# Optimization experiments

Hardware: AMD Instinct MI355X
Metric: run time of the kernel (lower is better)

Reference implementation:

```python
import jax, jax.numpy as jnp
import numpy as np

HEADS = 8
DIM_HEAD = 40
SCALE = DIM_HEAD ** -0.5


def setup_inputs() -> dict:
    key = jax.random.key(0)
    ks = jax.random.split(key, 6)
    B, S, D = 2, 4096, 320  # batch, seq (64x64 latent), query_dim
    inner = HEADS * DIM_HEAD  # 320
    s = 0.02
    return {
        "x": jax.random.normal(ks[0], (B, S, D), jnp.float32),
        "Wq": jax.random.normal(ks[1], (inner, D), jnp.float32) * s,
        "Wk": jax.random.normal(ks[2], (inner, D), jnp.float32) * s,
        "Wv": jax.random.normal(ks[3], (inner, D), jnp.float32) * s,
        "Wout": jax.random.normal(ks[4], (D, inner), jnp.float32) * s,
        "bout": jnp.zeros((D,), jnp.float32),
    }


def _split_heads(t):
    # [B, S, h*d] -> [B, h, S, d]
    B, S, _ = t.shape
    return t.reshape(B, S, HEADS, DIM_HEAD).transpose(0, 2, 1, 3)


def reference(x, Wq, Wk, Wv, Wout, bout):
    # self-attention path (context=None): k/v come from x
    q = _split_heads(x @ Wq.T)  # [B,h,S,d]
    k = _split_heads(x @ Wk.T)
    v = _split_heads(x @ Wv.T)
    # scores: materialized O(S^2) attention as in the torch einsum
    attn = jax.nn.softmax(jnp.einsum('bhid,bhjd->bhij', q, k) * SCALE, axis=-1)
    out = jnp.einsum('bhij,bhjd->bhid', attn, v)  # [B,h,S,d]
    B, _, S, _ = out.shape
    out = out.transpose(0, 2, 1, 3).reshape(B, S, HEADS * DIM_HEAD)
    return out @ Wout.T + bout  # to_out (dropout=0 -> identity)
```

## Files before the change

kernel.cpp:

```cpp
#include <hip/hip_runtime.h>

#define HEADS 8
#define DHEAD 40
#define SEQ   4096
#define BATCH 2
#define INNER 320
#define NBH   16
#define QSCALE ((float)(0.15811388300841897 * 1.4426950408889634))

typedef _Float16 f16;
typedef __attribute__((ext_vector_type(2)))  __fp16   fp16x2;
typedef __attribute__((ext_vector_type(4)))  _Float16 half4;
typedef __attribute__((ext_vector_type(8)))  _Float16 half8;
typedef __attribute__((ext_vector_type(16))) float    f32x16;

#if __has_builtin(__builtin_amdgcn_exp2f)
#define EXP2F(x) __builtin_amdgcn_exp2f(x)
#else
#define EXP2F(x) exp2f(x)
#endif

#define MFMA16(a, b, c) __builtin_amdgcn_mfma_f32_32x32x16_f16(a, b, c, 0, 0, 0)

union H8 { half8 h8; fp16x2 p2[4]; uint4 u4; };

#define WQKV4 (3 * INNER * INNER / 4)
#define WOUT4 (INNER * INNER / 4)
#define WTOT4 (WQKV4 + WOUT4)

__global__ __launch_bounds__(256)
void convert_kernel(const float* __restrict__ Wq,
                    const float* __restrict__ Wk,
                    const float* __restrict__ Wv,
                    const float* __restrict__ Wout,
                    f16* __restrict__ wh, f16* __restrict__ wouth)
{
    int i = blockIdx.x * 256 + threadIdx.x;
    if (i >= WTOT4) return;
    float4 v;
    f16* dst;
    float sc = 1.0f;
    if (i < WQKV4) {
        if (i < 25600)      { v = ((const float4*)Wq)[i]; sc = QSCALE; }
        else if (i < 51200) { v = ((const float4*)Wk)[i - 25600]; }
        else                { v = ((const float4*)Wv)[i - 51200]; }
        dst = wh + 4 * (size_t)i;
    } else {
        int j = i - WQKV4;
        v = ((const float4*)Wout)[j];
        dst = wouth + 4 * (size_t)j;
    }
    H8 u;
    u.p2[0] = __builtin_amdgcn_cvt_pkrtz(v.x * sc, v.y * sc);
    u.p2[1] = __builtin_amdgcn_cvt_pkrtz(v.z * sc, v.w * sc);
    *(uint2*)dst = make_uint2(u.u4.x, u.u4.y);
}

#define QSTR 72

__global__ __launch_bounds__(256)
void qkv_gemm_kernel(const float* __restrict__ x, const f16* __restrict__ wh,
                     f16* __restrict__ q, f16* __restrict__ k,
                     f16* __restrict__ vt)
{
    __shared__ f16 lds[(64 + 192) * QSTR];
    f16* As = lds;
    f16* Bs = lds + 64 * QSTR;

    const int tid = threadIdx.x;
    const int nb0 = blockIdx.x * 64;
    const int m0  = blockIdx.y * 64;
    const int wave = tid >> 6, lane = tid & 63, m = lane & 31, half = lane >> 5;
    const int mw = wave >> 1, nw = wave & 1;

    f32x16 acc[3];
    #pragma unroll
    for (int i = 0; i < 16; i++) { acc[0][i] = 0.f; acc[1][i] = 0.f; acc[2][i] = 0.f; }

    for (int k0 = 0; k0 < 320; k0 += 64) {
        __syncthreads();
        #pragma unroll
        for (int u = 0; u < 2; u++) {
            int idx = tid + 256 * u;
            int r = idx >> 3, c8 = idx & 7;
            const float* xr = &x[(size_t)(m0 + r) * 320 + k0 + c8 * 8];
            float4 v0 = *(const float4*)xr;
            float4 v1 = *(const float4*)(xr + 4);
            H8 hh;
            hh.p2[0] = __builtin_amdgcn_cvt_pkrtz(v0.x, v0.y);
            hh.p2[1] = __builtin_amdgcn_cvt_pkrtz(v0.z, v0.w);
            hh.p2[2] = __builtin_amdgcn_cvt_pkrtz(v1.x, v1.y);
            hh.p2[3] = __builtin_amdgcn_cvt_pkrtz(v1.z, v1.w);
            *(uint4*)&As[r * QSTR + c8 * 8] = hh.u4;
        }
        #pragma unroll
        for (int u = 0; u < 6; u++) {
            int idx = tid + 256 * u;
            int r = idx >> 3, c8 = idx & 7;
            int wr = (r >> 6) * 320 + nb0 + (r & 63);
            *(uint4*)&Bs[r * QSTR + c8 * 8] =
                *(const uint4*)&wh[(size_t)wr * 320 + k0 + c8 * 8];
        }
        __syncthreads();
        #pragma unroll
        for (int c = 0; c < 4; c++) {
            half8 a = *(const half8*)&As[(mw * 32 + m) * QSTR + c * 16 + half * 8];
            #pragma unroll
            for (int t = 0; t < 3; t++) {
                half8 bf = *(const half8*)&Bs[(nw * 96 + t * 32 + m) * QSTR + c * 16 + half * 8];
                acc[t] = MFMA16(a, bf, acc[t]);
            }
        }
    }

    const int b = m0 >> 12, s0 = m0 & 4095;

    #pragma unroll
    for (int t = 0; t < 3; t++) {
        int st = nw * 3 + t;
        if (st < 4) {
            f16* dst = (st < 2) ? q : k;
            int col = nb0 + (st & 1) * 32 + m;
            int h  = (col * 205) >> 13;
            int dd = col - h * 40;
            #pragma unroll
            for (int reg = 0; reg < 16; reg++) {
                int crow = 4 * half + (reg & 3) + 8 * (reg >> 2);
                int mg = m0 + mw * 32 + crow;
                int bb = mg >> 12, s = mg & 4095;
                dst[((size_t)(bb * 8 + h) * SEQ + s) * DHEAD + dd] = (f16)acc[t][reg];
            }
        }
    }

    __syncthreads();
    f16* Ct = lds;
    if (nw == 1) {
        #pragma unroll
        for (int t = 1; t < 3; t++) {
            int vr0 = (t - 1) * 32 + m;
            #pragma unroll
            for (int g = 0; g < 4; g++) {
                half4 hh;
                hh.x = (f16)acc[t][4 * g + 0]; hh.y = (f16)acc[t][4 * g + 1];
                hh.z = (f16)acc[t][4 * g + 2]; hh.w = (f16)acc[t][4 * g + 3];
                *(half4*)&Ct[vr0 * QSTR + mw * 32 + 8 * g + 4 * half] = hh;
            }
        }
    }
    __syncthreads();
    #pragma unroll
    for (int u = 0; u < 4; u++) {
        int idx = tid + 256 * u;
        int rl = idx >> 4, c4 = idx & 15;
        int col = nb0 + rl;
        int h  = (col * 205) >> 13;
        int dd = col - h * 40;
        int w4 = c4 & 3;
        int c4p = (c4 & ~3) | ((w4 == 1) ? 2 : (w4 == 2) ? 1 : w4);
        *(uint2*)&vt[((size_t)(b * 8 + h) * DHEAD + dd) * SEQ + s0 + c4p * 4] =
            *(const uint2*)&Ct[rl * QSTR + c4 * 4];
    }
}

__global__ __launch_bounds__(512, 4)
void attn_kernel(const f16* __restrict__ q, const f16* __restrict__ k,
                 const f16* __restrict__ vt, f16* __restrict__ y)
{
    __shared__ __align__(16) unsigned char ldsbuf[49152];
    f16*   ldsh = (f16*)ldsbuf;
    float* ldsf = (float*)ldsbuf;

    const int tid = threadIdx.x;
    const int blk = blockIdx.x;
    const int xcd = blk & 7, slot = blk >> 3;
    const int bh = xcd * 2 + (slot >> 5), qt = slot & 31;
    const int b = bh >> 3, h = bh & 7;
    const int q0 = qt * 128;
    const int wave = tid >> 6, lane = tid & 63, m = lane & 31, half = lane >> 5;
    const int qp = wave >> 1, kh = wave & 1;
    const int x7 = m & 7;

    if (tid < 192) {
        int bsel = tid >> 6, r = tid & 63;
        *(uint4*)&ldsh[bsel * 8192 + r * 64 + 8 * (5 ^ (r & 7))] = make_uint4(0, 0, 0, 0);
    }
    {
        int idx = tid;
        #pragma unroll
        for (int pass = 0; pass < 2; pass++) {
            if (pass == 0 || tid < 64) {
                int bsel = idx / 192;
                int j = idx - bsel * 192;
                int r = 40 + (j >> 3), c = j & 7;
                uint4 val = (r == 40) ? make_uint4(0x3C003C00u, 0x3C003C00u, 0x3C003C00u, 0x3C003C00u)
                                      : make_uint4(0, 0, 0, 0);
                *(uint4*)&ldsh[bsel * 8192 + 4096 + r * 64 + 8 * (c ^ (r & 7))] = val;
            }
            idx = 512 + tid;
        }
    }

    half8 zero8;
    #pragma unroll
    for (int j = 0; j < 8; j++) zero8[j] = (f16)0.0f;

    half8 qa[3];
    {
        const f16* qb = q + ((size_t)bh * SEQ + q0 + qp * 32 + m) * DHEAD;
        qa[0] = *(const half8*)&qb[half * 8];
        qa[1] = *(const half8*)&qb[16 + half * 8];
        qa[2] = (half == 1) ? zero8 : *(const half8*)&qb[32];
    }

    f32x16 O0, O1;
    #pragma unroll
    for (int i = 0; i < 16; i++) { O0[i] = 0.f; O1[i] = 0.f; }

    const f16* kb = k  + (size_t)bh * SEQ * DHEAD;
    const f16* vb = vt + (size_t)bh * DHEAD * SEQ;

    const bool aIsK = (tid < 320);
    int adst, astep;
    const f16* aptr;
    if (aIsK) {
        int r = (tid * 205) >> 10, c = tid - r * 5;
        adst = r * 64 + 8 * (c ^ (r & 7));
        aptr = kb + (size_t)r * DHEAD + c * 8;
        astep = 64 * DHEAD;
    } else {
        int t = tid - 320;
        int r = t >> 3, c = t & 7;
        adst = 4096 + r * 64 + 8 * (c ^ (r & 7));
        aptr = vb + (size_t)r * SEQ + c * 8;
        astep = 64;
    }
    const bool hasB = (tid < 128);
    int bdst = 0;
    const f16* bptr = vb;
    if (hasB) {
        int t = 192 + tid;
        int r = t >> 3, c = t & 7;
        bdst = 4096 + r * 64 + 8 * (c ^ (r & 7));
        bptr = vb + (size_t)r * SEQ + c * 8;
    }

    uint4 sA = *(const uint4*)aptr;
    uint4 sB = make_uint4(0, 0, 0, 0);
    if (hasB) sB = *(const uint4*)bptr;

    H8 p0, p1;
    int stg  = 0;
    int stgv = 0;

    {
        *(uint4*)&ldsh[stg + adst] = sA;
        if (hasB) *(uint4*)&ldsh[stg + bdst] = sB;
        __syncthreads();
        aptr += astep; sA = *(const uint4*)aptr;
        if (hasB) { bptr += 64; sB = *(const uint4*)bptr; }

        half8 kf[3];
        #pragma unroll
        for (int c = 0; c < 3; c++)
            kf[c] = *(const half8*)&ldsh[stg + (kh * 32 + m) * 64 + 8 * ((2 * c + half) ^ x7)];
        f32x16 S;
        #pragma unroll
        for (int i = 0; i < 16; i++) S[i] = 0.f;
        __builtin_amdgcn_s_setprio(1);
        S = MFMA16(kf[0], qa[0], S);
        S = MFMA16(kf[1], qa[1], S);
        S = MFMA16(kf[2], qa[2], S);
        __builtin_amdgcn_s_setprio(0);
        #pragma unroll
        for (int g = 0; g < 4; g++) {
            p0.p2[g] = __builtin_amdgcn_cvt_pkrtz(EXP2F(S[2 * g]),     EXP2F(S[2 * g + 1]));
            p1.p2[g] = __builtin_amdgcn_cvt_pkrtz(EXP2F(S[8 + 2 * g]), EXP2F(S[9 + 2 * g]));
        }
        stg = 8192;
    }

    for (int j = 1; j < 64; ++j) {
        *(uint4*)&ldsh[stg + adst] = sA;
        if (hasB) *(uint4*)&ldsh[stg + bdst] = sB;

        {
            const f16* Vb = &ldsh[stgv + 4096];
            half8 vf[2][2];
            #pragma unroll
            for (int c = 0; c < 2; c++) {
                vf[c][0] = *(const half8*)&Vb[m * 64        + 8 * ((4 * kh + 2 * c + half) ^ x7)];
                vf[c][1] = *(const half8*)&Vb[(32 + m) * 64 + 8 * ((4 * kh + 2 * c + half) ^ x7)];
            }
            __builtin_amdgcn_s_setprio(1);
            O0 = MFMA16(p0.h8, vf[0][0], O0);
            O1 = MFMA16(p0.h8, vf[0][1], O1);
            O0 = MFMA16(p1.h8, vf[1][0], O0);
            O1 = MFMA16(p1.h8, vf[1][1], O1);
            __builtin_amdgcn_s_setprio(0);
        }

        __syncthreads();

        if (j < 63) {
            aptr += astep; sA = *(const uint4*)aptr;
            if (hasB) { bptr += 64; sB = *(const uint4*)bptr; }
        }

        half8 kf[3];
        #pragma unroll
        for (int c = 0; c < 3; c++)
            kf[c] = *(const half8*)&ldsh[stg + (kh * 32 + m) * 64 + 8 * ((2 * c + half) ^ x7)];
        f32x16 S;
        #pragma unroll
        for (int i = 0; i < 16; i++) S[i] = 0.f;
        __builtin_amdgcn_s_setprio(1);
        S = MFMA16(kf[0], qa[0], S);
        S = MFMA16(kf[1], qa[1], S);
        S = MFMA16(kf[2], qa[2], S);
        __builtin_amdgcn_s_setprio(0);

        #pragma unroll
        for (int g = 0; g < 4; g++) {
            p0.p2[g] = __builtin_amdgcn_cvt_pkrtz(EXP2F(S[2 * g]),     EXP2F(S[2 * g + 1]));
            p1.p2[g] = __builtin_amdgcn_cvt_pkrtz(EXP2F(S[8 + 2 * g]), EXP2F(S[9 + 2 * g]));
        }

        stgv = stg;
        stg = (stg == 16384) ? 0 : stg + 8192;
    }

    {
        const f16* Vb = &ldsh[stgv + 4096];
        half8 vf[2][2];
        #pragma unroll
        for (int c = 0; c < 2; c++) {
            vf[c][0] = *(const half8*)&Vb[m * 64        + 8 * ((4 * kh + 2 * c + half) ^ x7)];
            vf[c][1] = *(const half8*)&Vb[(32 + m) * 64 + 8 * ((4 * kh + 2 * c + half) ^ x7)];
        }
        O0 = MFMA16(p0.h8, vf[0][0], O0);
        O1 = MFMA16(p0.h8, vf[0][1], O1);
        O0 = MFMA16(p1.h8, vf[1][0], O0);
        O1 = MFMA16(p1.h8, vf[1][1], O1);
    }

    __syncthreads();
    if (kh == 1) {
        #pragma unroll
        for (int reg = 0; reg < 16; reg++) {
            int row = 4 * half + (reg & 3) + 8 * (reg >> 2);
            ldsf[(qp * 32 + row) * 66 + m]      = O0[reg];
            ldsf[(qp * 32 + row) * 66 + 32 + m] = O1[reg];
        }
    }
    __syncthreads();
    if (kh == 0) {
        #pragma unroll
        for (int reg = 0; reg < 16; reg++) {
            int row = 4 * half + (reg & 3) + 8 * (reg >> 2);
            O0[reg] += ldsf[(qp * 32 + row) * 66 + m];
            O1[reg] += ldsf[(qp * 32 + row) * 66 + 32 + m];
        }
        #pragma unroll
        for (int reg = 0; reg < 16; reg++) {
            float l = __shfl(O1[reg], 8 + 32 * half, 64);
            float rinv = 1.0f / l;
            int row = 4 * half + (reg & 3) + 8 * (reg >> 2);
            f16* yr = y + ((size_t)b * SEQ + q0 + qp * 32 + row) * INNER + h * DHEAD;
            yr[m] = (f16)(O0[reg] * rinv);
            if (m < 8) yr[32 + m] = (f16)(O1[reg] * rinv);
        }
    }
}

#define ASTR 72

__global__ __launch_bounds__(256)
void out_proj_kernel(const f16* __restrict__ y, const f16* __restrict__ wouth,
                     const float* __restrict__ bout, float* __restrict__ out)
{
    __shared__ f16 lds[(128 + 64) * ASTR];
    f16* As = lds;
    f16* Bs = lds + 128 * ASTR;

    const int tid = threadIdx.x;
    const int m0 = blockIdx.y * 128;
    const int n0 = blockIdx.x * 64;
    const int wave = tid >> 6, lane = tid & 63, m = lane & 31, half = lane >> 5;

    f32x16 acc[2];
    #pragma unroll
    for (int i = 0; i < 16; i++) { acc[0][i] = 0.f; acc[1][i] = 0.f; }

    for (int k0 = 0; k0 < 320; k0 += 64) {
        __syncthreads();
        #pragma unroll
        for (int u = 0; u < 4; u++) {
            int idx = tid + 256 * u;
            int r = idx >> 3, c8 = idx & 7;
            *(uint4*)&As[r * ASTR + c8 * 8] =
                *(const uint4*)&y[(size_t)(m0 + r) * 320 + k0 + c8 * 8];
        }
        #pragma unroll
        for (int u = 0; u < 2; u++) {
            int idx = tid + 256 * u;
            int r = idx >> 3, c8 = idx & 7;
            *(uint4*)&Bs[r * ASTR + c8 * 8] =
                *(const uint4*)&wouth[(size_t)(n0 + r) * 320 + k0 + c8 * 8];
        }
        __syncthreads();
        #pragma unroll
        for (int c = 0; c < 4; c++) {
            half8 a  = *(const half8*)&As[(wave * 32 + m) * ASTR + c * 16 + half * 8];
            half8 b0 = *(const half8*)&Bs[m * ASTR + c * 16 + half * 8];
            half8 b1 = *(const half8*)&Bs[(32 + m) * ASTR + c * 16 + half * 8];
            acc[0] = MFMA16(a, b0, acc[0]);
            acc[1] = MFMA16(a, b1, acc[1]);
        }
    }

    #pragma unroll
    for (int nt = 0; nt < 2; nt++) {
        int n = n0 + nt * 32 + m;
        float bias = bout[n];
        #pragma unroll
        for (int reg = 0; reg < 16; reg++) {
            int crow = 4 * half + (reg & 3) + 8 * (reg >> 2);
            out[(size_t)(m0 + wave * 32 + crow) * 320 + n] = acc[nt][reg] + bias;
        }
    }
}

extern "C" void kernel_launch(void* const* d_in, const int* in_sizes, int n_in,
                              void* d_out, int out_size, void* d_ws, size_t ws_size,
                              hipStream_t stream)
{
    const float* x    = (const float*)d_in[0];
    const float* Wq   = (const float*)d_in[1];
    const float* Wk   = (const float*)d_in[2];
    const float* Wv   = (const float*)d_in[3];
    const float* Wout = (const float*)d_in[4];
    const float* bout = (const float*)d_in[5];
    float* out = (float*)d_out;

    unsigned char* ws = (unsigned char*)d_ws;
    f16* wh    = (f16*)(ws);
    f16* wouth = (f16*)(ws +   614400);
    f16* qd    = (f16*)(ws +   819200);
    f16* kd    = (f16*)(ws +  6062080);
    f16* vtd   = (f16*)(ws + 11304960);
    f16* yd    = (f16*)(ws + 16547840);

    convert_kernel <<<400,          256, 0, stream>>>(Wq, Wk, Wv, Wout, wh, wouth);
    qkv_gemm_kernel<<<dim3(5, 128), 256, 0, stream>>>(x, wh, qd, kd, vtd);
    attn_kernel    <<<512,          512, 0, stream>>>(qd, kd, vtd, yd);
    out_proj_kernel<<<dim3(5, 64),  256, 0, stream>>>(yd, wouth, bout, out);
}
```

Measured before the change: 159.5 us.

## Fuse weight fp16 conversion into GEMM loaders and reorder attention loop

Removes the separate weight conversion kernel; the QKV and output projection GEMMs now load fp32 weights and convert to fp16 (with Q scaling) while staging into LDS. This drops one kernel launch and a workspace round-trip, but each block redundantly converts weights and reads twice the weight bytes. The attention main loop is reordered so the barrier follows the K/V store immediately and the QK^T MFMAs for the new tile are issued before the PV MFMAs of the previous tile, aiming to improve MFMA/exp overlap.

```diff
diff --git a/kernel.cpp b/kernel.cpp
--- a/kernel.cpp
+++ b/kernel.cpp
@@ -24,42 +24,24 @@
 
 union H8 { half8 h8; fp16x2 p2[4]; uint4 u4; };
 
-#define WQKV4 (3 * INNER * INNER / 4)
-#define WOUT4 (INNER * INNER / 4)
-#define WTOT4 (WQKV4 + WOUT4)
+static __device__ __forceinline__ uint4 cvt8(const float* __restrict__ p, float sc) {
+    float4 v0 = *(const float4*)p;
+    float4 v1 = *(const float4*)(p + 4);
+    H8 hh;
+    hh.p2[0] = __builtin_amdgcn_cvt_pkrtz(v0.x * sc, v0.y * sc);
+    hh.p2[1] = __builtin_amdgcn_cvt_pkrtz(v0.z * sc, v0.w * sc);
+    hh.p2[2] = __builtin_amdgcn_cvt_pkrtz(v1.x * sc, v1.y * sc);
+    hh.p2[3] = __builtin_amdgcn_cvt_pkrtz(v1.z * sc, v1.w * sc);
+    return hh.u4;
+}
+
+#define QSTR 72
 
 __global__ __launch_bounds__(256)
-void convert_kernel(const float* __restrict__ Wq,
-                    const float* __restrict__ Wk,
-                    const float* __restrict__ Wv,
-                    const float* __restrict__ Wout,
-                    f16* __restrict__ wh, f16* __restrict__ wouth)
-{
-    int i = blockIdx.x * 256 + threadIdx.x;
-    if (i >= WTOT4) return;
-    float4 v;
-    f16* dst;
-    float sc = 1.0f;
-    if (i < WQKV4) {
-        if (i < 25600)      { v = ((const float4*)Wq)[i]; sc = QSCALE; }
-        else if (i < 51200) { v = ((const float4*)Wk)[i - 25600]; }
-        else                { v = ((const float4*)Wv)[i - 51200]; }
-        dst = wh + 4 * (size_t)i;
-    } else {
-        int j = i - WQKV4;
-        v = ((const float4*)Wout)[j];
-        dst = wouth + 4 * (size_t)j;
-    }
-    H8 u;
-    u.p2[0] = __builtin_amdgcn_cvt_pkrtz(v.x * sc, v.y * sc);
-    u.p2[1] = __builtin_amdgcn_cvt_pkrtz(v.z * sc, v.w * sc);
-    *(uint2*)dst = make_uint2(u.u4.x, u.u4.y);
-}
-
-#define QSTR 72
-
-__global__ __launch_bounds__(256)
-void qkv_gemm_kernel(const float* __restrict__ x, const f16* __restrict__ wh,
+void qkv_gemm_kernel(const float* __restrict__ x,
+                     const float* __restrict__ Wq,
+                     const float* __restrict__ Wk,
+                     const float* __restrict__ Wv,
                      f16* __restrict__ q, f16* __restrict__ k,
                      f16* __restrict__ vt)
 {
@@ -73,6 +55,18 @@
     const int wave = tid >> 6, lane = tid & 63, m = lane & 31, half = lane >> 5;
     const int mw = wave >> 1, nw = wave & 1;
 
+    const int bc8 = tid & 7;
+    const float* bsrc[6];
+    int bdst[6];
+    #pragma unroll
+    for (int u = 0; u < 6; u++) {
+        int idx = tid + 256 * u;
+        int r = idx >> 3;
+        const float* W = (r < 64) ? Wq : (r < 128) ? Wk : Wv;
+        bsrc[u] = W + (size_t)(nb0 + (r & 63)) * 320 + bc8 * 8;
+        bdst[u] = r * QSTR + bc8 * 8;
+    }
+
     f32x16 acc[3];
     #pragma unroll
     for (int i = 0; i < 16; i++) { acc[0][i] = 0.f; acc[1][i] = 0.f; acc[2][i] = 0.f; }
@@ -83,24 +77,12 @@
         for (int u = 0; u < 2; u++) {
             int idx = tid + 256 * u;
             int r = idx >> 3, c8 = idx & 7;
-            const float* xr = &x[(size_t)(m0 + r) * 320 + k0 + c8 * 8];
-            float4 v0 = *(const float4*)xr;
-            float4 v1 = *(const float4*)(xr + 4);
-            H8 hh;
-            hh.p2[0] = __builtin_amdgcn_cvt_pkrtz(v0.x, v0.y);
-            hh.p2[1] = __builtin_amdgcn_cvt_pkrtz(v0.z, v0.w);
-            hh.p2[2] = __builtin_amdgcn_cvt_pkrtz(v1.x, v1.y);
-            hh.p2[3] = __builtin_amdgcn_cvt_pkrtz(v1.z, v1.w);
-            *(uint4*)&As[r * QSTR + c8 * 8] = hh.u4;
-        }
-        #pragma unroll
-        for (int u = 0; u < 6; u++) {
-            int idx = tid + 256 * u;
-            int r = idx >> 3, c8 = idx & 7;
-            int wr = (r >> 6) * 320 + nb0 + (r & 63);
-            *(uint4*)&Bs[r * QSTR + c8 * 8] =
-                *(const uint4*)&wh[(size_t)wr * 320 + k0 + c8 * 8];
-        }
+            *(uint4*)&As[r * QSTR + c8 * 8] =
+                cvt8(&x[(size_t)(m0 + r) * 320 + k0 + c8 * 8], 1.0f);
+        }
+        #pragma unroll
+        for (int u = 0; u < 6; u++)
+            *(uint4*)&Bs[bdst[u]] = cvt8(bsrc[u] + k0, (u < 2) ? QSCALE : 1.0f);
         __syncthreads();
         #pragma unroll
         for (int c = 0; c < 4; c++) {
@@ -283,6 +265,25 @@
     for (int j = 1; j < 64; ++j) {
         *(uint4*)&ldsh[stg + adst] = sA;
         if (hasB) *(uint4*)&ldsh[stg + bdst] = sB;
+        __syncthreads();
+
+        if (j < 63) {
+            aptr += astep; sA = *(const uint4*)aptr;
+            if (hasB) { bptr += 64; sB = *(const uint4*)bptr; }
+        }
+
+        half8 kf[3];
+        #pragma unroll
+        for (int c = 0; c < 3; c++)
+            kf[c] = *(const half8*)&ldsh[stg + (kh * 32 + m) * 64 + 8 * ((2 * c + half) ^ x7)];
+        f32x16 S;
+        #pragma unroll
+        for (int i = 0; i < 16; i++) S[i] = 0.f;
+        __builtin_amdgcn_s_setprio(1);
+        S = MFMA16(kf[0], qa[0], S);
+        S = MFMA16(kf[1], qa[1], S);
+        S = MFMA16(kf[2], qa[2], S);
+        __builtin_amdgcn_s_setprio(0);
 
         {
             const f16* Vb = &ldsh[stgv + 4096];
@@ -300,26 +301,6 @@
             __builtin_amdgcn_s_setprio(0);
         }
 
-        __syncthreads();
-
-        if (j < 63) {
-            aptr += astep; sA = *(const uint4*)aptr;
-            if (hasB) { bptr += 64; sB = *(const uint4*)bptr; }
-        }
-
-        half8 kf[3];
-        #pragma unroll
-        for (int c = 0; c < 3; c++)
-            kf[c] = *(const half8*)&ldsh[stg + (kh * 32 + m) * 64 + 8 * ((2 * c + half) ^ x7)];
-        f32x16 S;
-        #pragma unroll
-        for (int i = 0; i < 16; i++) S[i] = 0.f;
-        __builtin_amdgcn_s_setprio(1);
-        S = MFMA16(kf[0], qa[0], S);
-        S = MFMA16(kf[1], qa[1], S);
-        S = MFMA16(kf[2], qa[2], S);
-        __builtin_amdgcn_s_setprio(0);
-
         #pragma unroll
         for (int g = 0; g < 4; g++) {
             p0.p2[g] = __builtin_amdgcn_cvt_pkrtz(EXP2F(S[2 * g]),     EXP2F(S[2 * g + 1]));
@@ -376,7 +357,7 @@
 #define ASTR 72
 
 __global__ __launch_bounds__(256)
-void out_proj_kernel(const f16* __restrict__ y, const f16* __restrict__ wouth,
+void out_proj_kernel(const f16* __restrict__ y, const float* __restrict__ Wout,
                      const float* __restrict__ bout, float* __restrict__ out)
 {
     __shared__ f16 lds[(128 + 64) * ASTR];
@@ -388,6 +369,17 @@
     const int n0 = blockIdx.x * 64;
     const int wave = tid >> 6, lane = tid & 63, m = lane & 31, half = lane >> 5;
 
+    const int bc8 = tid & 7;
+    const float* bsrc[2];
+    int bdst[2];
+    #pragma unroll
+    for (int u = 0; u < 2; u++) {
+        int idx = tid + 256 * u;
+        int r = idx >> 3;
+        bsrc[u] = Wout + (size_t)(n0 + r) * 320 + bc8 * 8;
+        bdst[u] = r * ASTR + bc8 * 8;
+    }
+
     f32x16 acc[2];
     #pragma unroll
     for (int i = 0; i < 16; i++) { acc[0][i] = 0.f; acc[1][i] = 0.f; }
@@ -402,12 +394,8 @@
                 *(const uint4*)&y[(size_t)(m0 + r) * 320 + k0 + c8 * 8];
         }
         #pragma unroll
-        for (int u = 0; u < 2; u++) {
-            int idx = tid + 256 * u;
-            int r = idx >> 3, c8 = idx & 7;
-            *(uint4*)&Bs[r * ASTR + c8 * 8] =
-                *(const uint4*)&wouth[(size_t)(n0 + r) * 320 + k0 + c8 * 8];
-        }
+        for (int u = 0; u < 2; u++)
+            *(uint4*)&Bs[bdst[u]] = cvt8(bsrc[u] + k0, 1.0f);
         __syncthreads();
         #pragma unroll
         for (int c = 0; c < 4; c++) {
@@ -444,15 +432,12 @@
     float* out = (float*)d_out;
 
     unsigned char* ws = (unsigned char*)d_ws;
-    f16* wh    = (f16*)(ws);
-    f16* wouth = (f16*)(ws +   614400);
-    f16* qd    = (f16*)(ws +   819200);
-    f16* kd    = (f16*)(ws +  6062080);
-    f16* vtd   = (f16*)(ws + 11304960);
-    f16* yd    = (f16*)(ws + 16547840);
-
-    convert_kernel <<<400,          256, 0, stream>>>(Wq, Wk, Wv, Wout, wh, wouth);
-    qkv_gemm_kernel<<<dim3(5, 128), 256, 0, stream>>>(x, wh, qd, kd, vtd);
+    f16* qd    = (f16*)(ws);
+    f16* kd    = (f16*)(ws +  5242880);
+    f16* vtd   = (f16*)(ws + 10485760);
+    f16* yd    = (f16*)(ws + 15728640);
+
+    qkv_gemm_kernel<<<dim3(5, 128), 256, 0, stream>>>(x, Wq, Wk, Wv, qd, kd, vtd);
     attn_kernel    <<<512,          512, 0, stream>>>(qd, kd, vtd, yd);
-    out_proj_kernel<<<dim3(5, 64),  256, 0, stream>>>(yd, wouth, bout, out);
+    out_proj_kernel<<<dim3(5, 64),  256, 0, stream>>>(yd, Wout, bout, out);
 }
```

Result: slower. 164.0 us (+2.8%).
